# Kernel optimization log

Hardware: AMD Instinct MI355X
Metric: run time of the kernel (lower is better)

## Reference

```python
import jax, jax.numpy as jnp
import numpy as np

EPS = 1e-5   # torch F.layer_norm default eps
TOP_K = 20   # int(3*D^2 / (2*hr*N^2 + 10*D)) for D=768, N=196, hr=1.0
NUM_EXPERTS = 200  # 10 * TOP_K


def setup_inputs() -> dict:
    key = jax.random.key(0)
    ks = jax.random.split(key, 6)
    B, N, D = 32, 196, 768
    E, H = NUM_EXPERTS, 196  # H = int(N * hidden_ratio)
    s = 0.02
    return {
        "x": jax.random.normal(ks[0], (B, N, D), jnp.float32),
        "Wr": jax.random.normal(ks[1], (E, D), jnp.float32) * s,   # router.weight
        "W1": jax.random.normal(ks[2], (E, H, N), jnp.float32) * s,  # fc1.weight per expert
        "b1": jnp.zeros((E, H), jnp.float32),
        "W2": jax.random.normal(ks[3], (E, N, H), jnp.float32) * s,  # fc2.weight per expert
        "b2": jnp.zeros((E, N), jnp.float32),
        "Wo": jax.random.normal(ks[4], (D, D), jnp.float32) * s,     # out_proj.weight
        "bo": jnp.zeros((D,), jnp.float32),
    }


def reference(x, Wr, W1, b1, W2, b2, Wo, bo):
    B, N, D = x.shape
    E = Wr.shape[0]
    K = TOP_K

    # Router: per-sample routing on token-mean features
    logits = x.mean(axis=1) @ Wr.T                      # (B, E)
    probs = jax.nn.softmax(logits, axis=-1)             # (B, E)
    w, idx = jax.lax.top_k(probs, K)                    # (B, K) sorted desc, as torch.topk
    w = w / w.sum(axis=-1, keepdims=True)               # renormalize top-k weights

    # TokenMixer operates in (B, D, N) space: layernorm over tokens (no affine),
    # then fc1 (N->H), gelu(tanh), fc2 (H->N).
    xt = jnp.swapaxes(x, 1, 2)                          # (B, D, N)
    mu = xt.mean(axis=-1, keepdims=True)
    var = xt.var(axis=-1, keepdims=True)                # population var (matches F.layer_norm)
    z = (xt - mu) * jax.lax.rsqrt(var + EPS)            # (B, D, N)

    # Gather each sample's K expert weight matrices and batch the MLPs.
    W1g, b1g = W1[idx], b1[idx]                         # (B,K,H,N), (B,K,H)
    W2g, b2g = W2[idx], b2[idx]                         # (B,K,N,H), (B,K,N)

    h = jnp.einsum('bdn,bkhn->bkdh', z, W1g) + b1g[:, :, None, :]
    a = jax.nn.gelu(h, approximate=True)                # tanh-approx GELU
    o = jnp.einsum('bkdh,bknh->bkdn', a, W2g) + b2g[:, :, None, :]

    # Weighted combine over the K selected experts, back to (B, N, D)
    mix = jnp.einsum('bk,bkdn->bnd', w, o)

    out = mix @ Wo.T + bo                               # out_proj

    # Load-balancing aux loss (top-1 assignment fraction vs mean router prob)
    top1 = jax.nn.one_hot(idx[:, 0], E, dtype=probs.dtype)   # (B, E)
    aux = E * jnp.sum(probs.mean(axis=0) * top1.mean(axis=0))
    return out, aux
```

## Files before the change

### kernel.cpp

```cpp
#include <hip/hip_runtime.h>
#include <math.h>

constexpr int B  = 32;
constexpr int N  = 196;
constexpr int D  = 768;
constexpr int E  = 200;
constexpr int TK = 20;

constexpr int NGRP = 4;
constexpr int PRB  = 14336;
constexpr int EXB  = 114688;
constexpr int LK   = 40;

typedef __bf16 bf16x8 __attribute__((ext_vector_type(8)));
typedef __bf16 bf16x4 __attribute__((ext_vector_type(4)));
typedef float  f32x4  __attribute__((ext_vector_type(4)));
typedef long   longx2 __attribute__((ext_vector_type(2)));
typedef unsigned char uchar;

#define GLDS16(gp, lp)                                                        \
  __builtin_amdgcn_global_load_lds(                                           \
      (const __attribute__((address_space(1))) void*)(gp),                    \
      (__attribute__((address_space(3))) void*)(lp), 16, 0, 0)

#define WAITVM12  __builtin_amdgcn_s_waitcnt(0x0F7C)
#define WAITVM8   __builtin_amdgcn_s_waitcnt(0x0F78)
#define WAITVM0   __builtin_amdgcn_s_waitcnt(0x0F70)
#define WAITLGKM0 __builtin_amdgcn_s_waitcnt(0xC07F)
#define BAR       __builtin_amdgcn_s_barrier()

__device__ __forceinline__ float gelu_fast(float x) {
  float u = x * fmaf(x * x, 0.044715f, 1.0f);
  float e = exp2f(-2.3022084f * u);
  return x * __builtin_amdgcn_rcpf(1.0f + e);
}

__device__ __forceinline__ uchar f32_to_f8(float v) {
  return (uchar)(__builtin_amdgcn_cvt_pk_fp8_f32(v, v, 0, false) & 0xff);
}

__global__ __launch_bounds__(256) void k_ln(const float* __restrict__ x,
                                            uchar* __restrict__ zb,
                                            float* __restrict__ mu) {
  int b = blockIdx.x / 12, dt = blockIdx.x % 12;
  int d0 = dt * 64;
  int t = threadIdx.x;
  int q = t >> 6, d = t & 63;
  __shared__ float ps[256], pq[256];
  __shared__ float ms[64], rss[64];
  __shared__ alignas(16) uchar zt[64 * 256];

  for (int i = t; i < 1024; i += 256) ((uint4*)zt)[i] = (uint4){0, 0, 0, 0};

  const float* xp = x + ((size_t)b * N + q * 49) * D + d0 + d;
  float v[49];
  float s = 0.f, sq = 0.f;
  #pragma unroll
  for (int n = 0; n < 49; ++n) {
    v[n] = xp[(size_t)n * D];
    s += v[n]; sq += v[n] * v[n];
  }
  ps[t] = s; pq[t] = sq;
  __syncthreads();
  if (t < 64) {
    float S = ps[t] + ps[t + 64] + ps[t + 128] + ps[t + 192];
    float Q = pq[t] + pq[t + 64] + pq[t + 128] + pq[t + 192];
    float m = S * (1.0f / N);
    float var = Q * (1.0f / N) - m * m;
    ms[t] = m; rss[t] = rsqrtf(var + 1e-5f);
    mu[(size_t)b * D + d0 + t] = m;
  }
  __syncthreads();
  float m = ms[d], r = rss[d];
  int dsw = (d >> 1) & 3;
  #pragma unroll
  for (int n = 0; n < 49; ++n) {
    int tok = q * 49 + n;
    int qp = ((tok >> 3) & 3) ^ dsw;
    int off = d * 256 + (tok >> 6) * 64 + qp * 16 + ((tok >> 5) & 1) * 8 + (tok & 7);
    zt[off] = f32_to_f8((v[n] - m) * r);
  }
  __syncthreads();
  #pragma unroll
  for (int pair = 0; pair < 4; ++pair) {
    uint4* dst = (uint4*)(zb + (((size_t)b * 4 + pair) * 768 + d0) * 64);
    dst[t] = ((const uint4*)zt)[(t >> 2) * 16 + pair * 4 + (t & 3)];
  }
}

__global__ __launch_bounds__(256) void k_prep(
    const float* __restrict__ W1, const float* __restrict__ W2,
    const float* __restrict__ Wo,
    uchar* __restrict__ Wf, __bf16* __restrict__ Wob,
    const float* __restrict__ mu, const float* __restrict__ Wr,
    float* __restrict__ probs, int* __restrict__ idxg,
    float* __restrict__ wg) {
  int bx = blockIdx.x;
  int t = threadIdx.x;
  __shared__ alignas(16) uchar ls[224 * 256];
  __shared__ float sp[E];
  __shared__ float smax, ssum;
  __shared__ float svals[TK];
  __shared__ int   sidx[TK];

  if (bx >= 976) {
    int b = bx - 976;
    int lane = t & 63, wave = t >> 6;
    float* smu = (float*)ls;
    for (int i = t; i < 768; i += 256) smu[i] = mu[(size_t)b * D + i];
    __syncthreads();
    const float4* m4 = (const float4*)smu;
    #pragma unroll 1
    for (int i = 0; i < 50; ++i) {
      int e = wave * 50 + i;
      const float4* wr4 = (const float4*)(Wr + (size_t)e * D);
      float acc = 0.f;
      #pragma unroll
      for (int j = 0; j < 3; ++j) {
        float4 w = wr4[lane + j * 64], mm = m4[lane + j * 64];
        acc = fmaf(w.x, mm.x, acc); acc = fmaf(w.y, mm.y, acc);
        acc = fmaf(w.z, mm.z, acc); acc = fmaf(w.w, mm.w, acc);
      }
      #pragma unroll
      for (int off = 32; off > 0; off >>= 1) acc += __shfl_down(acc, off);
      if (lane == 0) sp[e] = acc;
    }
    __syncthreads();
    if (t < 64) {
      float mx = -1e30f;
      for (int e = t; e < E; e += 64) mx = fmaxf(mx, sp[e]);
      #pragma unroll
      for (int off = 32; off > 0; off >>= 1) mx = fmaxf(mx, __shfl_down(mx, off));
      if (t == 0) smax = mx;
    }
    __syncthreads();
    if (t < E) sp[t] = exp2f((sp[t] - smax) * 1.44269504f);
    __syncthreads();
    if (t < 64) {
      float s = 0.f;
      for (int e = t; e < E; e += 64) s += sp[e];
      #pragma unroll
      for (int off = 32; off > 0; off >>= 1) s += __shfl_down(s, off);
      if (t == 0) ssum = s;
    }
    __syncthreads();
    if (t < E) {
      sp[t] = sp[t] / ssum;
      probs[(size_t)b * E + t] = sp[t];
    }
    __syncthreads();
    for (int k = 0; k < TK; ++k) {
      if (t < 64) {
        float bv = -1e30f; int bi = 0;
        for (int e = t; e < E; e += 64) {
          float v = sp[e];
          if (v > bv) { bv = v; bi = e; }
        }
        #pragma unroll
        for (int off = 32; off > 0; off >>= 1) {
          float ov = __shfl_down(bv, off);
          int   oi = __shfl_down(bi, off);
          if (ov > bv || (ov == bv && oi < bi)) { bv = ov; bi = oi; }
        }
        if (t == 0) {
          svals[k] = bv; sidx[k] = bi;
          sp[bi] = -2e30f;
        }
      }
      __syncthreads();
    }
    if (t == 0) {
      float s = 0.f;
      for (int k = 0; k < TK; ++k) s += svals[k];
      float inv = 1.0f / s;
      for (int k = 0; k < TK; ++k) {
        wg[b * TK + k]   = svals[k] * inv;
        idxg[b * TK + k] = sidx[k];
      }
    }
    return;
  }

  if (bx >= 400) {
    int i = (bx - 400) * 256 + t;
    float4 v = *(const float4*)&Wo[(size_t)i * 4];
    bf16x4 o = {(__bf16)v.x, (__bf16)v.y, (__bf16)v.z, (__bf16)v.w};
    *(bf16x4*)&Wob[(size_t)i * 4] = o;
    return;
  }
  int e = bx >> 1, mat = bx & 1;
  for (int i = t; i < 3584; i += 256) ((uint4*)ls)[i] = (uint4){0, 0, 0, 0};
  __syncthreads();
  const float* src = (mat ? W2 : W1) + (size_t)e * 196 * 196;
  for (int i = t; i < 196 * 49; i += 256) {
    int r = i / 49, c4 = (i - r * 49) * 4;
    float4 v = *(const float4*)&src[(size_t)r * 196 + c4];
    int lo = __builtin_amdgcn_cvt_pk_fp8_f32(v.x, v.y, 0, false);
    unsigned int pk = (unsigned int)__builtin_amdgcn_cvt_pk_fp8_f32(v.z, v.w, lo, true);
    *(unsigned int*)&ls[r * 256 + c4] = pk;
  }
  __syncthreads();
  uchar* dst = Wf + (size_t)e * EXB + mat * 4 * PRB;
  for (int s = t; s < 3584; s += 256) {
    int p = s / 896, rem = s - p * 896;
    int col = rem >> 2, qp = rem & 3;
    int ql = qp ^ ((col >> 1) & 3);
    unsigned long lo = *(const unsigned long*)&ls[col * 256 + p * 64 + ql * 8];
    unsigned long hi = *(const unsigned long*)&ls[col * 256 + p * 64 + 32 + ql * 8];
    longx2 o; o[0] = (long)lo; o[1] = (long)hi;
    *(longx2*)&dst[(size_t)s * 16] = o;
  }
}

__global__ __launch_bounds__(256, 2) void k_expert(
    const uchar* __restrict__ zb, const uchar* __restrict__ Wf,
    const float* __restrict__ b1, const float* __restrict__ b2,
    const int* __restrict__ idxg, const float* __restrict__ wg,
    __bf16* __restrict__ mixg) {
  __shared__ alignas(16) uchar pool[75776];
  __shared__ alignas(16) __bf16 b1s[5 * 196];
  __shared__ float bsum_s[196];
  __shared__ int   eidx_s[5];
  __shared__ float w_s[5];
  uchar* zs  = pool;
  uchar* at  = pool + 16384;
  uchar* wsb = pool + 32768;
  __bf16* tb = (__bf16*)pool;

  int xw = blockIdx.x & 7, rr_ = blockIdx.x >> 3;
  int j = rr_ / 12, dt = rr_ - j * 12;
  int gid = j * 8 + xw;
  int g = gid & 3, b = gid >> 2;
  int d0 = dt * 64;

  int t = threadIdx.x;
  int lane = t & 63, wave = t >> 6;
  int quad = lane >> 4, l16 = lane & 15;
  int wrow = (wave & 1) * 32;
  int wcol = (wave >> 1) * 112;
  int qp = quad ^ ((l16 >> 1) & 3);

  if (t < 5) {
    eidx_s[t] = idxg[b * TK + g * 5 + t];
    w_s[t]    = wg[b * TK + g * 5 + t];
  }
  for (int i = t; i < 980; i += 256) {
    int kk = i / 196, col = i - kk * 196;
    int ee = idxg[b * TK + g * 5 + kk];
    b1s[i] = (__bf16)b1[ee * 196 + col];
  }
  if (t < 196) {
    float s = 0.f;
    #pragma unroll
    for (int k5 = 0; k5 < 5; ++k5) {
      int ee = idxg[b * TK + g * 5 + k5];
      s += wg[b * TK + g * 5 + k5] * b2[ee * 196 + t];
    }
    bsum_s[t] = s;
  }
  __syncthreads();

  {
    const uchar* zbase = zb + ((size_t)b * 4 * 768 + d0) * 64;
    #pragma unroll
    for (int p = 0; p < 4; ++p)
      GLDS16(zbase + (size_t)p * (768 * 64) + t * 16, zs + p * 4096 + t * 16);
  }

  int s0 = t * 16, s1 = (t + 256) * 16, s2 = (t + 512) * 16;
  int s3 = ((t & 127) + 768) * 16;

  auto issue = [&](int qn) {
    int qq = qn > 39 ? 39 : qn;
    int kk2 = qq >> 3, rem = qq & 7;
    const uchar* src = Wf + (size_t)eidx_s[kk2] * EXB + rem * PRB;
    int bi = qn & 3;
    uchar* lb = (bi == 3) ? pool : wsb + bi * PRB;
    GLDS16(src + s0, lb + s0);
    GLDS16(src + s1, lb + s1);
    GLDS16(src + s2, lb + s2);
    GLDS16(src + s3, lb + s3);
  };
  issue(0); issue(1); issue(2);

  WAITVM12;
  BAR;
  const uchar* zbase_l = zs + (wrow + l16) * 64 + qp * 16;
  longx2 zf[3][2];
  #pragma unroll
  for (int p = 0; p < 3; ++p) {
    zf[p][0] = *(const longx2*)(zbase_l + p * 4096);
    zf[p][1] = *(const longx2*)(zbase_l + p * 4096 + 1024);
  }
  long z3r0 = *(const long*)(zbase_l + 3 * 4096);
  long z3r1 = *(const long*)(zbase_l + 3 * 4096 + 1024);

  const uchar* abase = at + (wrow + l16) * 64 + qp * 16;

  f32x4 macc[14];
  #pragma unroll
  for (int i = 0; i < 14; ++i) macc[i] = (f32x4){0.f, 0.f, 0.f, 0.f};

  #pragma unroll 1
  for (int kk = 0; kk < 5; ++kk) {
    float wkv = w_s[kk];
    f32x4 hacc[14];
    #pragma unroll
    for (int i = 0; i < 14; ++i) hacc[i] = (f32x4){0.f, 0.f, 0.f, 0.f};

    #pragma unroll 1
    for (int p = 0; p < 3; ++p) {
      int q = kk * 8 + p;
      WAITVM8;
      BAR;
      int bi = q & 3;
      const uchar* buf = (bi == 3) ? pool : wsb + bi * PRB;
      const uchar* bb = buf + (wcol + l16) * 64 + qp * 16;
      __builtin_amdgcn_s_setprio(1);
      #pragma unroll
      for (int ct = 0; ct < 7; ++ct) {
        longx2 bf = *(const longx2*)(bb + ct * 1024);
        hacc[ct]     = __builtin_amdgcn_mfma_f32_16x16x32_fp8_fp8(bf[0], zf[p][0][0], hacc[ct], 0, 0, 0);
        hacc[ct]     = __builtin_amdgcn_mfma_f32_16x16x32_fp8_fp8(bf[1], zf[p][0][1], hacc[ct], 0, 0, 0);
        hacc[7 + ct] = __builtin_amdgcn_mfma_f32_16x16x32_fp8_fp8(bf[0], zf[p][1][0], hacc[7 + ct], 0, 0, 0);
        hacc[7 + ct] = __builtin_amdgcn_mfma_f32_16x16x32_fp8_fp8(bf[1], zf[p][1][1], hacc[7 + ct], 0, 0, 0);
      }
      __builtin_amdgcn_s_setprio(0);
      issue(q + 3);
    }
    {
      int q = kk * 8 + 3;
      WAITVM8;
      BAR;
      int bi = q & 3;
      const uchar* buf = (bi == 3) ? pool : wsb + bi * PRB;
      const uchar* bb = buf + (wcol + l16) * 64 + qp * 16;
      __builtin_amdgcn_s_setprio(1);
      #pragma unroll
      for (int ct = 0; ct < 7; ++ct) {
        long bf0 = *(const long*)(bb + ct * 1024);
        hacc[ct]     = __builtin_amdgcn_mfma_f32_16x16x32_fp8_fp8(bf0, z3r0, hacc[ct], 0, 0, 0);
        hacc[7 + ct] = __builtin_amdgcn_mfma_f32_16x16x32_fp8_fp8(bf0, z3r1, hacc[7 + ct], 0, 0, 0);
      }
      __builtin_amdgcn_s_setprio(0);
      issue(q + 3);
    }

    #pragma unroll
    for (int ct = 0; ct < 7; ++ct) {
      int hb = wcol + ct * 16 + quad * 4;
      bool valid = hb < 196;
      unsigned pk0 = 0u, pk1 = 0u;
      if (valid) {
        bf16x4 b4 = *(const bf16x4*)&b1s[kk * 196 + hb];
        float bv0 = (float)b4[0], bv1 = (float)b4[1];
        float bv2 = (float)b4[2], bv3 = (float)b4[3];
        f32x4 h0 = hacc[ct], h1 = hacc[7 + ct];
        pk0 = (unsigned)__builtin_amdgcn_cvt_pk_fp8_f32(
                  gelu_fast(h0[0] + bv0) * wkv, gelu_fast(h0[1] + bv1) * wkv, 0, false);
        pk0 = (unsigned)__builtin_amdgcn_cvt_pk_fp8_f32(
                  gelu_fast(h0[2] + bv2) * wkv, gelu_fast(h0[3] + bv3) * wkv, (int)pk0, true);
        pk1 = (unsigned)__builtin_amdgcn_cvt_pk_fp8_f32(
                  gelu_fast(h1[0] + bv0) * wkv, gelu_fast(h1[1] + bv1) * wkv, 0, false);
        pk1 = (unsigned)__builtin_amdgcn_cvt_pk_fp8_f32(
                  gelu_fast(h1[2] + bv2) * wkv, gelu_fast(h1[3] + bv3) * wkv, (int)pk1, true);
      }
      int d0r = wrow + l16;
      int addr0 = (hb >> 6) * 4096 + d0r * 64 + ((((hb >> 3) & 3) ^ ((d0r >> 1) & 3)) << 4)
                + ((hb >> 5) & 1) * 8 + (quad & 1) * 4;
      *(unsigned*)&at[addr0]        = pk0;
      *(unsigned*)&at[addr0 + 1024] = pk1;
    }
    WAITLGKM0;

    #pragma unroll 1
    for (int p = 0; p < 3; ++p) {
      int q = kk * 8 + 4 + p;
      WAITVM8;
      BAR;
      int bi = q & 3;
      const uchar* buf = (bi == 3) ? pool : wsb + bi * PRB;
      const uchar* bb = buf + (wcol + l16) * 64 + qp * 16;
      longx2 a0 = *(const longx2*)(abase + p * 4096);
      longx2 a1 = *(const longx2*)(abase + p * 4096 + 1024);
      __builtin_amdgcn_s_setprio(1);
      #pragma unroll
      for (int ct = 0; ct < 7; ++ct) {
        longx2 bf = *(const longx2*)(bb + ct * 1024);
        macc[ct]     = __builtin_amdgcn_mfma_f32_16x16x32_fp8_fp8(a0[0], bf[0], macc[ct], 0, 0, 0);
        macc[ct]     = __builtin_amdgcn_mfma_f32_16x16x32_fp8_fp8(a0[1], bf[1], macc[ct], 0, 0, 0);
        macc[7 + ct] = __builtin_amdgcn_mfma_f32_16x16x32_fp8_fp8(a1[0], bf[0], macc[7 + ct], 0, 0, 0);
        macc[7 + ct] = __builtin_amdgcn_mfma_f32_16x16x32_fp8_fp8(a1[1], bf[1], macc[7 + ct], 0, 0, 0);
      }
      __builtin_amdgcn_s_setprio(0);
      issue(q + 3);
    }
    {
      int q = kk * 8 + 7;
      WAITVM8;
      BAR;
      int bi = q & 3;
      const uchar* buf = (bi == 3) ? pool : wsb + bi * PRB;
      const uchar* bb = buf + (wcol + l16) * 64 + qp * 16;
      long a0h = *(const long*)(abase + 3 * 4096);
      long a1h = *(const long*)(abase + 3 * 4096 + 1024);
      __builtin_amdgcn_s_setprio(1);
      #pragma unroll
      for (int ct = 0; ct < 7; ++ct) {
        long bf0 = *(const long*)(bb + ct * 1024);
        macc[ct]     = __builtin_amdgcn_mfma_f32_16x16x32_fp8_fp8(a0h, bf0, macc[ct], 0, 0, 0);
        macc[7 + ct] = __builtin_amdgcn_mfma_f32_16x16x32_fp8_fp8(a1h, bf0, macc[7 + ct], 0, 0, 0);
      }
      __builtin_amdgcn_s_setprio(0);
      issue(q + 3);
    }
  }

  WAITVM0;
  BAR;
  #pragma unroll
  for (int ct = 0; ct < 7; ++ct) {
    int ncol = wcol + ct * 16 + l16;
    float bsum = (ncol < 196) ? bsum_s[ncol] : 0.f;
    #pragma unroll
    for (int rt = 0; rt < 2; ++rt) {
      f32x4 v = macc[rt * 7 + ct];
      bf16x4 o = {(__bf16)(v[0] + bsum), (__bf16)(v[1] + bsum),
                  (__bf16)(v[2] + bsum), (__bf16)(v[3] + bsum)};
      *(bf16x4*)&tb[ncol * 68 + wrow + rt * 16 + quad * 4] = o;
    }
  }
  __syncthreads();
  __bf16* mp = mixg + ((size_t)(g * B + b) * N) * D + d0;
  #pragma unroll
  for (int i = 0; i < 7; ++i) {
    int s = i * 256 + t;
    if (s < 1568) {
      int n = s >> 3, c = s & 7;
      const uint2* pa = (const uint2*)&tb[n * 68 + c * 8];
      uint2 v0 = pa[0], v1 = pa[1];
      uint4 v = {v0.x, v0.y, v1.x, v1.y};
      *(uint4*)&mp[(size_t)n * D + c * 8] = v;
    }
  }
}

__global__ __launch_bounds__(256, 2) void k_outproj(
    const __bf16* __restrict__ mixg, const __bf16* __restrict__ Wob,
    const float* __restrict__ bo, const float* __restrict__ probs,
    const int* __restrict__ idxg, float* __restrict__ out,
    float* __restrict__ out_aux) {
  __shared__ alignas(16) __bf16 As[32 * LK];
  __shared__ alignas(16) __bf16 Bs[256 * LK];
  const size_t GS = (size_t)B * N * D;

  int t = threadIdx.x;
  if (blockIdx.x == 0 && t < 32) {
    int top1 = idxg[t * TK];
    float s = 0.f;
    for (int bb = 0; bb < B; ++bb) s += probs[(size_t)bb * E + top1];
    #pragma unroll
    for (int off = 16; off > 0; off >>= 1) s += __shfl_down(s, off);
    if (t == 0) out_aux[0] = s * ((float)E / ((float)B * (float)B));
  }

  int m0 = (blockIdx.x % 196) * 32;
  int e0 = (blockIdx.x / 196) * 256;
  int lane = t & 63, wave = t >> 6;
  int quad = lane >> 4, l16 = lane & 15;
  int wrow = (wave & 1) * 16;
  int wcol = (wave >> 1) * 128;
  int arow = t >> 2, ach = t & 3;
  const __bf16* ap0 = mixg + (size_t)(m0 + (arow & 31)) * D + ach * 8;

  f32x4 acc[8];
  #pragma unroll
  for (int i = 0; i < 8; ++i) acc[i] = (f32x4){0.f, 0.f, 0.f, 0.f};

  const uint4* wsrc = (const uint4*)Wob;
  #pragma unroll 1
  for (int c = 0; c < 24; ++c) {
    int k0 = c * 32;
    __syncthreads();
    if (t < 128) {
      const __bf16* ap = ap0 + k0;
      bf16x8 g0 = *(const bf16x8*)(ap);
      bf16x8 g1 = *(const bf16x8*)(ap + GS);
      bf16x8 g2 = *(const bf16x8*)(ap + 2 * GS);
      bf16x8 g3 = *(const bf16x8*)(ap + 3 * GS);
      bf16x8 r;
      #pragma unroll
      for (int jj = 0; jj < 8; ++jj)
        r[jj] = (__bf16)((float)g0[jj] + (float)g1[jj] + (float)g2[jj] + (float)g3[jj]);
      *(bf16x8*)&As[arow * LK + ach * 8] = r;
    }
    for (int p = t; p < 1024; p += 256) {
      int rr = p >> 2, sub = p & 3;
      uint4 v = wsrc[(((size_t)(e0 + rr)) * D + k0) / 8 + sub];
      *(uint4*)&Bs[rr * LK + sub * 8] = v;
    }
    __syncthreads();
    bf16x8 a0 = *(const bf16x8*)&As[(wrow + l16) * LK + quad * 8];
    #pragma unroll
    for (int ct = 0; ct < 8; ++ct) {
      bf16x8 bfr = *(const bf16x8*)&Bs[(wcol + ct * 16 + l16) * LK + quad * 8];
      acc[ct] = __builtin_amdgcn_mfma_f32_16x16x32_bf16(a0, bfr, acc[ct], 0, 0, 0);
    }
  }

  #pragma unroll
  for (int ct = 0; ct < 8; ++ct) {
    int e = e0 + wcol + ct * 16 + l16;
    float bov = bo[e];
    #pragma unroll
    for (int rx = 0; rx < 4; ++rx) {
      int m = m0 + wrow + quad * 4 + rx;
      out[(size_t)m * D + e] = acc[ct][rx] + bov;
    }
  }
}

extern "C" void kernel_launch(void* const* d_in, const int* in_sizes, int n_in,
                              void* d_out, int out_size, void* d_ws, size_t ws_size,
                              hipStream_t stream) {
  const float* x  = (const float*)d_in[0];
  const float* Wr = (const float*)d_in[1];
  const float* W1 = (const float*)d_in[2];
  const float* b1 = (const float*)d_in[3];
  const float* W2 = (const float*)d_in[4];
  const float* b2 = (const float*)d_in[5];
  const float* Wo = (const float*)d_in[6];
  const float* bo = (const float*)d_in[7];
  float* out = (float*)d_out;

  char* p = (char*)d_ws;
  auto alloc = [&](size_t bytes) {
    char* r = p;
    p += (bytes + 255) & ~(size_t)255;
    return r;
  };
  uchar*  zb   = (uchar*)alloc((size_t)B * 4 * 768 * 64);
  float*  mu   = (float*)alloc((size_t)B * D * 4);
  uchar*  Wf   = (uchar*)alloc((size_t)E * EXB);
  __bf16* Wob  = (__bf16*)alloc((size_t)D * D * 2);
  __bf16* mixg = (__bf16*)alloc((size_t)NGRP * B * N * D * 2);
  float*  probs= (float*)alloc((size_t)B * E * 4);
  int*    idxg = (int*)alloc((size_t)B * TK * 4);
  float*  wg   = (float*)alloc((size_t)B * TK * 4);

  k_ln<<<dim3(B * 12), dim3(256), 0, stream>>>(x, zb, mu);
  k_prep<<<dim3(1008), dim3(256), 0, stream>>>(W1, W2, Wo, Wf, Wob,
                                               mu, Wr, probs, idxg, wg);
  k_expert<<<dim3(1536), dim3(256), 0, stream>>>(zb, Wf, b1, b2, idxg, wg, mixg);
  k_outproj<<<dim3(588), dim3(256), 0, stream>>>(mixg, Wob, bo, probs, idxg,
                                                 out, out + (size_t)B * N * D);
}
```

Baseline: 349.0 us.

## Split expert weight prep into halves, widen tail LDS loads, raise outproj occupancy

```diff
diff --git a/kernel.cpp b/kernel.cpp
--- a/kernel.cpp
+++ b/kernel.cpp
@@ -28,6 +28,8 @@
 #define WAITVM0   __builtin_amdgcn_s_waitcnt(0x0F70)
 #define WAITLGKM0 __builtin_amdgcn_s_waitcnt(0xC07F)
 #define BAR       __builtin_amdgcn_s_barrier()
+
+#define KEEP64(v) asm volatile("" : : "v"(v))
 
 __device__ __forceinline__ float gelu_fast(float x) {
   float u = x * fmaf(x * x, 0.044715f, 1.0f);
@@ -97,14 +99,14 @@
     float* __restrict__ wg) {
   int bx = blockIdx.x;
   int t = threadIdx.x;
-  __shared__ alignas(16) uchar ls[224 * 256];
+  __shared__ alignas(16) uchar ls[112 * 256];
   __shared__ float sp[E];
   __shared__ float smax, ssum;
   __shared__ float svals[TK];
   __shared__ int   sidx[TK];
 
-  if (bx >= 976) {
-    int b = bx - 976;
+  if (bx >= 1376) {
+    int b = bx - 1376;
     int lane = t & 63, wave = t >> 6;
     float* smu = (float*)ls;
     for (int i = t; i < 768; i += 256) smu[i] = mu[(size_t)b * D + i];
@@ -181,34 +183,38 @@
     return;
   }
 
-  if (bx >= 400) {
-    int i = (bx - 400) * 256 + t;
+  if (bx >= 800) {
+    int i = (bx - 800) * 256 + t;
     float4 v = *(const float4*)&Wo[(size_t)i * 4];
     bf16x4 o = {(__bf16)v.x, (__bf16)v.y, (__bf16)v.z, (__bf16)v.w};
     *(bf16x4*)&Wob[(size_t)i * 4] = o;
     return;
   }
-  int e = bx >> 1, mat = bx & 1;
-  for (int i = t; i < 3584; i += 256) ((uint4*)ls)[i] = (uint4){0, 0, 0, 0};
+
+  int e = bx >> 2, mat = (bx >> 1) & 1, half = bx & 1;
+  int r0 = half * 112;
+  int nrows = half ? 84 : 112;
+  for (int i = t; i < 1792; i += 256) ((uint4*)ls)[i] = (uint4){0, 0, 0, 0};
   __syncthreads();
   const float* src = (mat ? W2 : W1) + (size_t)e * 196 * 196;
-  for (int i = t; i < 196 * 49; i += 256) {
-    int r = i / 49, c4 = (i - r * 49) * 4;
-    float4 v = *(const float4*)&src[(size_t)r * 196 + c4];
+  for (int i = t; i < nrows * 49; i += 256) {
+    int rl = i / 49, c4 = (i - rl * 49) * 4;
+    float4 v = *(const float4*)&src[(size_t)(r0 + rl) * 196 + c4];
     int lo = __builtin_amdgcn_cvt_pk_fp8_f32(v.x, v.y, 0, false);
     unsigned int pk = (unsigned int)__builtin_amdgcn_cvt_pk_fp8_f32(v.z, v.w, lo, true);
-    *(unsigned int*)&ls[r * 256 + c4] = pk;
+    *(unsigned int*)&ls[rl * 256 + c4] = pk;
   }
   __syncthreads();
   uchar* dst = Wf + (size_t)e * EXB + mat * 4 * PRB;
-  for (int s = t; s < 3584; s += 256) {
-    int p = s / 896, rem = s - p * 896;
-    int col = rem >> 2, qp = rem & 3;
+  for (int s = t; s < 1792; s += 256) {
+    int p = s / 448, rem = s - p * 448;
+    int cl = rem >> 2, qp = rem & 3;
+    int col = r0 + cl;
     int ql = qp ^ ((col >> 1) & 3);
-    unsigned long lo = *(const unsigned long*)&ls[col * 256 + p * 64 + ql * 8];
-    unsigned long hi = *(const unsigned long*)&ls[col * 256 + p * 64 + 32 + ql * 8];
+    unsigned long lo = *(const unsigned long*)&ls[cl * 256 + p * 64 + ql * 8];
+    unsigned long hi = *(const unsigned long*)&ls[cl * 256 + p * 64 + 32 + ql * 8];
     longx2 o; o[0] = (long)lo; o[1] = (long)hi;
-    *(longx2*)&dst[(size_t)s * 16] = o;
+    *(longx2*)&dst[(size_t)(p * 896 + col * 4 + qp) * 16] = o;
   }
 }
 
@@ -292,8 +298,13 @@
     zf[p][0] = *(const longx2*)(zbase_l + p * 4096);
     zf[p][1] = *(const longx2*)(zbase_l + p * 4096 + 1024);
   }
-  long z3r0 = *(const long*)(zbase_l + 3 * 4096);
-  long z3r1 = *(const long*)(zbase_l + 3 * 4096 + 1024);
+  long z3r0, z3r1;
+  {
+    longx2 zt0 = *(const longx2*)(zbase_l + 3 * 4096);
+    longx2 zt1 = *(const longx2*)(zbase_l + 3 * 4096 + 1024);
+    KEEP64(zt0[1]); KEEP64(zt1[1]);
+    z3r0 = zt0[0]; z3r1 = zt1[0];
+  }
 
   const uchar* abase = at + (wrow + l16) * 64 + qp * 16;
 
@@ -338,9 +349,10 @@
       __builtin_amdgcn_s_setprio(1);
       #pragma unroll
       for (int ct = 0; ct < 7; ++ct) {
-        long bf0 = *(const long*)(bb + ct * 1024);
-        hacc[ct]     = __builtin_amdgcn_mfma_f32_16x16x32_fp8_fp8(bf0, z3r0, hacc[ct], 0, 0, 0);
-        hacc[7 + ct] = __builtin_amdgcn_mfma_f32_16x16x32_fp8_fp8(bf0, z3r1, hacc[7 + ct], 0, 0, 0);
+        longx2 bf = *(const longx2*)(bb + ct * 1024);
+        KEEP64(bf[1]);
+        hacc[ct]     = __builtin_amdgcn_mfma_f32_16x16x32_fp8_fp8(bf[0], z3r0, hacc[ct], 0, 0, 0);
+        hacc[7 + ct] = __builtin_amdgcn_mfma_f32_16x16x32_fp8_fp8(bf[0], z3r1, hacc[7 + ct], 0, 0, 0);
       }
       __builtin_amdgcn_s_setprio(0);
       issue(q + 3);
@@ -402,14 +414,20 @@
       int bi = q & 3;
       const uchar* buf = (bi == 3) ? pool : wsb + bi * PRB;
       const uchar* bb = buf + (wcol + l16) * 64 + qp * 16;
-      long a0h = *(const long*)(abase + 3 * 4096);
-      long a1h = *(const long*)(abase + 3 * 4096 + 1024);
+      long a0h, a1h;
+      {
+        longx2 at0 = *(const longx2*)(abase + 3 * 4096);
+        longx2 at1 = *(const longx2*)(abase + 3 * 4096 + 1024);
+        KEEP64(at0[1]); KEEP64(at1[1]);
+        a0h = at0[0]; a1h = at1[0];
+      }
       __builtin_amdgcn_s_setprio(1);
       #pragma unroll
       for (int ct = 0; ct < 7; ++ct) {
-        long bf0 = *(const long*)(bb + ct * 1024);
-        macc[ct]     = __builtin_amdgcn_mfma_f32_16x16x32_fp8_fp8(a0h, bf0, macc[ct], 0, 0, 0);
-        macc[7 + ct] = __builtin_amdgcn_mfma_f32_16x16x32_fp8_fp8(a1h, bf0, macc[7 + ct], 0, 0, 0);
+        longx2 bf = *(const longx2*)(bb + ct * 1024);
+        KEEP64(bf[1]);
+        macc[ct]     = __builtin_amdgcn_mfma_f32_16x16x32_fp8_fp8(a0h, bf[0], macc[ct], 0, 0, 0);
+        macc[7 + ct] = __builtin_amdgcn_mfma_f32_16x16x32_fp8_fp8(a1h, bf[0], macc[7 + ct], 0, 0, 0);
       }
       __builtin_amdgcn_s_setprio(0);
       issue(q + 3);
@@ -445,7 +463,7 @@
   }
 }
 
-__global__ __launch_bounds__(256, 2) void k_outproj(
+__global__ __launch_bounds__(256, 4) void k_outproj(
     const __bf16* __restrict__ mixg, const __bf16* __restrict__ Wob,
     const float* __restrict__ bo, const float* __restrict__ probs,
     const int* __restrict__ idxg, float* __restrict__ out,
@@ -549,7 +567,7 @@
   float*  wg   = (float*)alloc((size_t)B * TK * 4);
 
   k_ln<<<dim3(B * 12), dim3(256), 0, stream>>>(x, zb, mu);
-  k_prep<<<dim3(1008), dim3(256), 0, stream>>>(W1, W2, Wo, Wf, Wob,
+  k_prep<<<dim3(1408), dim3(256), 0, stream>>>(W1, W2, Wo, Wf, Wob,
                                                mu, Wr, probs, idxg, wg);
   k_expert<<<dim3(1536), dim3(256), 0, stream>>>(zb, Wf, b1, b2, idxg, wg, mixg);
   k_outproj<<<dim3(588), dim3(256), 0, stream>>>(mixg, Wob, bo, probs, idxg,
```

Measured after the change: 349.7 us. About the same (+0.2%).
